# Optimization experiments

Hardware: AMD Instinct MI355X
Metric: run time of the kernel (lower is better)

## Reference

```python
import jax, jax.numpy as jnp
import numpy as np

FG_FRACTION = 0.5
FG_THRESH = 0.7
BG_HI = 0.5
BG_LO = 0.1
BATCHSIZE = 256
FG_ROIS = int(round(FG_FRACTION * BATCHSIZE))  # 128


def setup_inputs() -> dict:
    key = jax.random.key(0)
    k1, k2, k3 = jax.random.split(key, 3)
    N, K, C = 80000, 256, 81
    IMG = 800.0

    def make_boxes(k, n):
        ka, kb = jax.random.split(k)
        xy = jax.random.uniform(ka, (1, n, 2), dtype=jnp.float32) * (IMG - 136.0)
        wh = jax.random.uniform(kb, (1, n, 2), dtype=jnp.float32) * 128.0 + 8.0
        return jnp.concatenate([xy, xy + wh], axis=-1)  # valid x1<x2, y1<y2

    proposals = make_boxes(k1, N)          # (1, N, 4)
    gt_boxes = make_boxes(k2, K)           # (1, K, 4)
    cls = jax.random.randint(k3, (K,), 1, C)
    gt_labels = jax.nn.one_hot(cls, C, dtype=jnp.float32)[None]  # (1, K, C)
    return {"proposals": proposals, "gt_labels": gt_labels, "gt_boxes": gt_boxes}


def _iou(a, b):
    # a: (M,4), b: (K,4); keras_rcnn +1-pixel convention
    area_a = (a[:, 2] - a[:, 0] + 1.0) * (a[:, 3] - a[:, 1] + 1.0)
    area_b = (b[:, 2] - b[:, 0] + 1.0) * (b[:, 3] - b[:, 1] + 1.0)
    x1 = jnp.maximum(a[:, None, 0], b[None, :, 0])
    y1 = jnp.maximum(a[:, None, 1], b[None, :, 1])
    x2 = jnp.minimum(a[:, None, 2], b[None, :, 2])
    y2 = jnp.minimum(a[:, None, 3], b[None, :, 3])
    iw = jnp.maximum(x2 - x1 + 1.0, 0.0)
    ih = jnp.maximum(y2 - y1 + 1.0, 0.0)
    inter = iw * ih  # (M, K)
    return inter / (area_a[:, None] + area_b[None, :] - inter)


def _bbox_transform(ex, gt):
    ew = ex[:, 2] - ex[:, 0] + 1.0
    eh = ex[:, 3] - ex[:, 1] + 1.0
    ecx = ex[:, 0] + 0.5 * ew
    ecy = ex[:, 1] + 0.5 * eh
    gw = gt[:, 2] - gt[:, 0] + 1.0
    gh = gt[:, 3] - gt[:, 1] + 1.0
    gcx = gt[:, 0] + 0.5 * gw
    gcy = gt[:, 1] + 0.5 * gh
    return jnp.stack([(gcx - ecx) / ew, (gcy - ecy) / eh,
                      jnp.log(gw / ew), jnp.log(gh / eh)], axis=1)  # (B, 4)


def _forward(proposals, gt_labels, gt_boxes):
    all_rois = jnp.concatenate([proposals[0], gt_boxes[0]], axis=0)  # (M, 4)
    gt_b = gt_boxes[0]    # (K, 4)
    gt_l = gt_labels[0]   # (K, C)
    C = gt_l.shape[1]

    ov = _iou(all_rois, gt_b)               # (M, K)
    gt_assign = jnp.argmax(ov, axis=1)      # (M,)
    max_ov = jnp.max(ov, axis=1)            # (M,)

    fg_mask = max_ov >= FG_THRESH
    bg_mask = (max_ov < BG_HI) & (max_ov >= BG_LO)

    M = all_rois.shape[0]
    order = jnp.arange(M)
    # deterministic stand-in for random shuffle: candidates first, in index order
    fg_sorted = jnp.argsort(jnp.where(fg_mask, order, M + order))
    bg_sorted = jnp.argsort(jnp.where(bg_mask, order, M + order))
    num_fg = jnp.sum(fg_mask.astype(jnp.int32))
    fg_take = jnp.minimum(FG_ROIS, num_fg)

    pos = jnp.arange(BATCHSIZE)
    is_fg_slot = pos < fg_take
    keep = jnp.where(is_fg_slot,
                     fg_sorted[jnp.clip(pos, 0, M - 1)],
                     bg_sorted[jnp.clip(pos - fg_take, 0, M - 1)])  # (B,)

    rois = all_rois[keep]                    # (B, 4)
    labels = gt_l[gt_assign[keep]]           # (B, C)
    # set_label_background: bg slots -> one-hot class 0
    bg_onehot = jax.nn.one_hot(0, C, dtype=labels.dtype)
    labels = jnp.where(is_fg_slot[:, None], labels, bg_onehot[None, :])

    assigned_gt = gt_b[gt_assign[keep]]      # (B, 4)
    targets = _bbox_transform(rois, assigned_gt)  # (B, 4)

    # expand to N x 4K: only the argmax class (if > 0) gets nonzero targets
    clss = jnp.argmax(labels, axis=1)        # (B,)
    cls_oh = jnp.where((clss > 0)[:, None],
                       jax.nn.one_hot(clss, C, dtype=targets.dtype), 0.0)  # (B, C)
    bbox_targets = (cls_oh[:, :, None] * targets[:, None, :]).reshape(BATCHSIZE, 4 * C)

    return rois[None], labels[None], bbox_targets[None]


def reference(proposals, gt_labels, gt_boxes):
    return _forward(proposals, gt_labels, gt_boxes)
```

## Files before the change

kernel.cpp:

```cpp
#include <hip/hip_runtime.h>

#define FG_THRESH 0.7f
#define BG_HI 0.5f
#define BG_LO 0.1f
#define BATCH 256
#define FG_ROIS 128
#define KGT 256
#define CLS 81
#define CPT 5
#define NCHPAD 1280
#define NBIN 26
#define NSPAN 6

typedef unsigned long long ull;

__global__ __launch_bounds__(256) void k_iou(
    const float* __restrict__ proposals,
    const float* __restrict__ gt_boxes,
    int N, int M, int NCH,
    int* __restrict__ gt_assign,
    ull* __restrict__ fgm,
    ull* __restrict__ bgm,
    ull* __restrict__ nbm)
{
    __shared__ float4 gshE[KGT];
    __shared__ float garea[KGT];
    __shared__ ull pbx[4][NBIN], pby[4][NBIN];
    __shared__ ull intX[4][NBIN][NSPAN], intY[4][NBIN][NSPAN];
    __shared__ unsigned int wm[3][4];

    int tid = threadIdx.x;
    int wv = tid >> 6, lane = tid & 63;

    float4 g = ((const float4*)gt_boxes)[tid];
    gshE[tid] = g;
    garea[tid] = (g.z - g.x + 1.0f) * (g.w - g.y + 1.0f);

    for (int b = 0; b < NBIN; ++b) {
        float hiE = 32.0f * (float)(b + 1);
        float loE = 32.0f * (float)b - 1.0f;
        ull mx = __ballot((g.x < hiE) && (g.z > loE));
        ull my = __ballot((g.y < hiE) && (g.w > loE));
        if (lane == 0) { pbx[wv][b] = mx; pby[wv][b] = my; }
    }
    __syncthreads();

    if (tid < 104) {
        int c = tid / NBIN, b = tid % NBIN;
        ull m = pbx[c][b];
        intX[c][b][0] = m;
        #pragma unroll
        for (int s = 1; s < NSPAN; ++s) {
            int bb = b + s;
            if (bb < NBIN) m |= pbx[c][bb];
            intX[c][b][s] = m;
        }
    } else if (tid >= 128 && tid < 232) {
        int u = tid - 128;
        int c = u / NBIN, b = u % NBIN;
        ull m = pby[c][b];
        intY[c][b][0] = m;
        #pragma unroll
        for (int s = 1; s < NSPAN; ++s) {
            int bb = b + s;
            if (bb < NBIN) m |= pby[c][bb];
            intY[c][b][s] = m;
        }
    }
    __syncthreads();

    int c = lane & 3;
    int rj = lane >> 2;

    for (int p = 0; p < 2; ++p) {
        int ch = blockIdx.x * 2 + p;
        if (ch >= NCH) break;
        int roi = ch * 64 + wv * 16 + rj;
        bool val = (roi < M);

        float4 a;
        if (val) a = (roi < N) ? ((const float4*)proposals)[roi] : gshE[roi - N];
        else     a = gshE[0];
        float az1 = a.z + 1.0f, aw1 = a.w + 1.0f;
        float area_a = (a.z - a.x + 1.0f) * (a.w - a.y + 1.0f);

        int b1x = (int)(a.x * 0.03125f);
        int b2x = (int)(az1 * 0.03125f);
        int b1y = (int)(a.y * 0.03125f);
        int b2y = (int)(aw1 * 0.03125f);
        b2x = min(b2x, NBIN - 1); b2y = min(b2y, NBIN - 1);
        int sx = b2x - b1x;
        int sy = b2y - b1y;

        ull mbits = val ? (intX[c][b1x][sx] & intY[c][b1y][sy]) : 0ull;

        float best = 0.0f;
        int bestk = 0;
        while (mbits) {
            int j = __ffsll(mbits) - 1;
            mbits &= mbits - 1;
            int k = (c << 6) + j;
            float4 gg = gshE[k];
            float x1 = fmaxf(a.x, gg.x);
            float y1 = fmaxf(a.y, gg.y);
            float x2 = fminf(a.z, gg.z);
            float y2 = fminf(a.w, gg.w);
            float iw = fmaxf(x2 - x1 + 1.0f, 0.0f);
            float ih = fmaxf(y2 - y1 + 1.0f, 0.0f);
            float inter = iw * ih;
            float q = inter / (area_a + garea[k] - inter);
            if (q > best) { best = q; bestk = k; }
        }

        #pragma unroll
        for (int d = 1; d < 4; d <<= 1) {
            float ob = __shfl_xor(best, d);
            int   kb = __shfl_xor(bestk, d);
            if (ob > best || (ob == best && kb < bestk)) { best = ob; bestk = kb; }
        }
        float bset = __shfl(best, (lane & 15) * 4);
        int   bk   = __shfl(bestk, (lane & 15) * 4);

        int roi2 = ch * 64 + wv * 16 + (lane & 15);
        bool isv = (lane < 16) && (roi2 < M);
        bool fgp = isv && (bset >= FG_THRESH);
        bool bgp = isv && (bset < BG_HI) && (bset >= BG_LO);
        bool nbp = isv && !bgp;
        if (isv) gt_assign[roi2] = bk;

        unsigned int mf = (unsigned int)(__ballot(fgp) & 0xFFFFull);
        unsigned int mb = (unsigned int)(__ballot(bgp) & 0xFFFFull);
        unsigned int mn = (unsigned int)(__ballot(nbp) & 0xFFFFull);
        if (lane == 0) { wm[0][wv] = mf; wm[1][wv] = mb; wm[2][wv] = mn; }
        __syncthreads();
        if (tid == 0) {
            fgm[ch] = (ull)wm[0][0] | ((ull)wm[0][1] << 16) | ((ull)wm[0][2] << 32) | ((ull)wm[0][3] << 48);
            bgm[ch] = (ull)wm[1][0] | ((ull)wm[1][1] << 16) | ((ull)wm[1][2] << 32) | ((ull)wm[1][3] << 48);
            nbm[ch] = (ull)wm[2][0] | ((ull)wm[2][1] << 16) | ((ull)wm[2][2] << 32) | ((ull)wm[2][3] << 48);
        }
        __syncthreads();
    }
}

__global__ __launch_bounds__(256) void k_finish(
    const float* __restrict__ proposals,
    const float* __restrict__ gt_boxes,
    const float* __restrict__ gt_labels,
    int N, int NCH,
    const int* __restrict__ gt_assign,
    const ull* __restrict__ fgm,
    const ull* __restrict__ bgm,
    const ull* __restrict__ nbm,
    float* __restrict__ out_rois,
    float* __restrict__ out_labels,
    float4* __restrict__ out_bbox)
{
    __shared__ ull sf[NCHPAD], sb[NCHPAD], sn[NCHPAD];
    __shared__ int pf[NCHPAD], pb[NCHPAD], pn[NCHPAD];
    __shared__ int fgl[FG_ROIS], bgl[BATCH], nbl[BATCH];
    __shared__ int wtot[3][4];
    __shared__ int lm_cls[8];
    __shared__ float4 lm_t[8];

    int tid = threadIdx.x;
    int lane = tid & 63, wv = tid >> 6;

    for (int idx = tid; idx < NCHPAD; idx += 256) {
        bool v = (idx < NCH);
        sf[idx] = v ? fgm[idx] : 0ull;
        sb[idx] = v ? bgm[idx] : 0ull;
    }
    __syncthreads();

    int lo = tid * CPT;
    int pc0 = 0, pc1 = 0;
    #pragma unroll
    for (int r = 0; r < CPT; ++r) {
        pc0 += __popcll(sf[lo + r]);
        pc1 += __popcll(sb[lo + r]);
    }
    int i0 = pc0, i1 = pc1;
    #pragma unroll
    for (int d = 1; d < 64; d <<= 1) {
        int t0 = __shfl_up(i0, d);
        int t1 = __shfl_up(i1, d);
        if (lane >= d) { i0 += t0; i1 += t1; }
    }
    if (lane == 63) { wtot[0][wv] = i0; wtot[1][wv] = i1; }
    __syncthreads();
    int o0 = 0, o1 = 0;
    for (int x = 0; x < wv; ++x) { o0 += wtot[0][x]; o1 += wtot[1][x]; }
    int b0 = o0 + i0 - pc0;
    int b1 = o1 + i1 - pc1;
    int num_fg = wtot[0][0] + wtot[0][1] + wtot[0][2] + wtot[0][3];
    int num_bg = wtot[1][0] + wtot[1][1] + wtot[1][2] + wtot[1][3];
    int fg_take = min(FG_ROIS, num_fg);
    bool need_nb = (fg_take + num_bg < BATCH);

    #pragma unroll
    for (int r = 0; r < CPT; ++r) {
        int w = lo + r;
        pf[w] = b0; b0 += __popcll(sf[w]);
        pb[w] = b1; b1 += __popcll(sb[w]);
    }
    __syncthreads();

    #pragma unroll
    for (int pass = 0; pass < CPT; ++pass) {
        int w = tid + 256 * pass;
        int base = pf[w];
        if (base < FG_ROIS) {
            ull m = sf[w];
            while (m) {
                if (base >= FG_ROIS) break;
                fgl[base++] = (w << 6) + __ffsll(m) - 1;
                m &= m - 1;
            }
        }
        base = pb[w];
        if (base < BATCH) {
            ull m = sb[w];
            while (m) {
                if (base >= BATCH) break;
                bgl[base++] = (w << 6) + __ffsll(m) - 1;
                m &= m - 1;
            }
        }
    }

    if (need_nb) {
        for (int idx = tid; idx < NCHPAD; idx += 256) {
            sn[idx] = (idx < NCH) ? nbm[idx] : 0ull;
        }
        __syncthreads();
        int pc2 = 0;
        #pragma unroll
        for (int r = 0; r < CPT; ++r) pc2 += __popcll(sn[lo + r]);
        int i2 = pc2;
        #pragma unroll
        for (int d = 1; d < 64; d <<= 1) {
            int t2 = __shfl_up(i2, d);
            if (lane >= d) i2 += t2;
        }
        if (lane == 63) wtot[2][wv] = i2;
        __syncthreads();
        int o2 = 0;
        for (int x = 0; x < wv; ++x) o2 += wtot[2][x];
        int b2 = o2 + i2 - pc2;
        #pragma unroll
        for (int r = 0; r < CPT; ++r) {
            int w = lo + r;
            pn[w] = b2; b2 += __popcll(sn[w]);
        }
        __syncthreads();
        #pragma unroll
        for (int pass = 0; pass < CPT; ++pass) {
            int w = tid + 256 * pass;
            int base = pn[w];
            if (base < BATCH) {
                ull m = sn[w];
                while (m) {
                    if (base >= BATCH) break;
                    nbl[base++] = (w << 6) + __ffsll(m) - 1;
                    m &= m - 1;
                }
            }
        }
    }
    __syncthreads();

    int eBase = blockIdx.x * 256;
    int posLo = eBase / CLS;
    int posHi = (eBase + 255) / CLS;
    int np = posHi - posLo + 1;

    for (int s = wv; s < np; s += 4) {
        int pos = posLo + s;
        int is_fg = (pos < fg_take) ? 1 : 0;
        int j = pos - fg_take;
        int keep = is_fg ? fgl[pos] : ((j < num_bg) ? bgl[j] : nbl[j - num_bg]);
        float4 a = (keep < N) ? ((const float4*)proposals)[keep]
                              : ((const float4*)gt_boxes)[keep - N];
        int ga = gt_assign[keep];
        float4 g = ((const float4*)gt_boxes)[ga];

        float ew = a.z - a.x + 1.0f, eh = a.w - a.y + 1.0f;
        float ecx = a.x + 0.5f * ew, ecy = a.y + 0.5f * eh;
        float gw = g.z - g.x + 1.0f, gh = g.w - g.y + 1.0f;
        float gcx = g.x + 0.5f * gw, gcy = g.y + 0.5f * gh;

        int cls = 0;
        if (is_fg) {
            float l1 = gt_labels[(size_t)ga * CLS + lane];
            int c2 = lane + 64;
            float l2 = (c2 < CLS) ? gt_labels[(size_t)ga * CLS + c2] : 0.0f;
            ull m1 = __ballot(l1 > 0.5f);
            ull m2 = __ballot(c2 < CLS && l2 > 0.5f);
            cls = m1 ? (__ffsll(m1) - 1) : (m2 ? 64 + __ffsll(m2) - 1 : 0);
        }
        if (lane == 0) {
            lm_cls[s] = cls;
            lm_t[s] = make_float4((gcx - ecx) / ew, (gcy - ecy) / eh,
                                  logf(gw / ew), logf(gh / eh));
        }
    }

    if (blockIdx.x == 0) {
        int pos = tid;
        int is_fg = (pos < fg_take) ? 1 : 0;
        int j = pos - fg_take;
        int keep = is_fg ? fgl[pos] : ((j < num_bg) ? bgl[j] : nbl[j - num_bg]);
        float4 a = (keep < N) ? ((const float4*)proposals)[keep]
                              : ((const float4*)gt_boxes)[keep - N];
        ((float4*)out_rois)[pos] = a;
    }
    __syncthreads();

    int e = eBase + tid;
    int pos = e / CLS, cc = e - pos * CLS;
    int li = pos - posLo;
    int cl = lm_cls[li];
    out_labels[e] = (cc == cl) ? 1.0f : 0.0f;
    out_bbox[e] = (cl > 0 && cc == cl) ? lm_t[li]
                                       : make_float4(0.f, 0.f, 0.f, 0.f);
}

extern "C" void kernel_launch(void* const* d_in, const int* in_sizes, int n_in,
                              void* d_out, int out_size, void* d_ws, size_t ws_size,
                              hipStream_t stream)
{
    const float* proposals = (const float*)d_in[0];
    const float* gt_labels = (const float*)d_in[1];
    const float* gt_boxes  = (const float*)d_in[2];
    int N = in_sizes[0] / 4;
    int K = in_sizes[2] / 4;
    int M = N + K;
    int NCH = (M + 63) / 64;

    char* ws = (char*)d_ws;
    size_t off = 0;
    auto alloc = [&](size_t bytes) -> void* {
        void* p = ws + off;
        off += (bytes + 255) & ~(size_t)255;
        return p;
    };
    int* gt_assign = (int*)alloc((size_t)M * 4);
    ull* fgm = (ull*)alloc((size_t)NCH * 8);
    ull* bgm = (ull*)alloc((size_t)NCH * 8);
    ull* nbm = (ull*)alloc((size_t)NCH * 8);

    float* out_rois   = (float*)d_out;
    float* out_labels = out_rois + BATCH * 4;
    float4* out_bbox  = (float4*)(out_labels + BATCH * CLS);

    int nb1 = (NCH + 1) / 2;
    k_iou<<<nb1, 256, 0, stream>>>(proposals, gt_boxes, N, M, NCH,
                                   gt_assign, fgm, bgm, nbm);
    int nb2 = (BATCH * CLS) / 256;
    k_finish<<<nb2, 256, 0, stream>>>(proposals, gt_boxes, gt_labels, N, NCH,
                                      gt_assign, fgm, bgm, nbm,
                                      out_rois, out_labels, out_bbox);
    (void)K; (void)n_in; (void)out_size; (void)ws_size;
}
```

Before: 26.39 us.

## Assign one ROI per lane and one chunk per wave in IoU kernel

The IoU kernel now gives each lane a whole ROI, looping over all four GT groups itself, instead of spreading each ROI over four lanes and merging with shuffles. Each wave handles one 64-ROI chunk and writes its fg/bg/nb masks straight from a ballot, which removes the shared-memory staging and both block barriers per chunk. The grid is a quarter of the chunk count rather than half, so there are fewer blocks and less per-block setup of the bin tables. In exchange, each lane runs a longer serial loop over candidates, and lanes in a wave may diverge more because candidate counts differ per ROI.

```diff
diff --git a/kernel.cpp b/kernel.cpp
--- a/kernel.cpp
+++ b/kernel.cpp
@@ -27,7 +27,6 @@
     __shared__ float garea[KGT];
     __shared__ ull pbx[4][NBIN], pby[4][NBIN];
     __shared__ ull intX[4][NBIN][NSPAN], intY[4][NBIN][NSPAN];
-    __shared__ unsigned int wm[3][4];
 
     int tid = threadIdx.x;
     int wv = tid >> 6, lane = tid & 63;
@@ -69,33 +68,35 @@
     }
     __syncthreads();
 
-    int c = lane & 3;
-    int rj = lane >> 2;
-
-    for (int p = 0; p < 2; ++p) {
-        int ch = blockIdx.x * 2 + p;
-        if (ch >= NCH) break;
-        int roi = ch * 64 + wv * 16 + rj;
-        bool val = (roi < M);
-
-        float4 a;
-        if (val) a = (roi < N) ? ((const float4*)proposals)[roi] : gshE[roi - N];
-        else     a = gshE[0];
-        float az1 = a.z + 1.0f, aw1 = a.w + 1.0f;
-        float area_a = (a.z - a.x + 1.0f) * (a.w - a.y + 1.0f);
-
-        int b1x = (int)(a.x * 0.03125f);
-        int b2x = (int)(az1 * 0.03125f);
-        int b1y = (int)(a.y * 0.03125f);
-        int b2y = (int)(aw1 * 0.03125f);
-        b2x = min(b2x, NBIN - 1); b2y = min(b2y, NBIN - 1);
-        int sx = b2x - b1x;
-        int sy = b2y - b1y;
-
-        ull mbits = val ? (intX[c][b1x][sx] & intY[c][b1y][sy]) : 0ull;
-
-        float best = 0.0f;
-        int bestk = 0;
+    int ch = blockIdx.x * 4 + wv;
+    if (ch >= NCH) return;
+    int roi = ch * 64 + lane;
+    bool isv = (roi < M);
+
+    float4 a;
+    if (isv) a = (roi < N) ? ((const float4*)proposals)[roi] : gshE[roi - N];
+    else     a = gshE[0];
+    float az1 = a.z + 1.0f, aw1 = a.w + 1.0f;
+    float area_a = (a.z - a.x + 1.0f) * (a.w - a.y + 1.0f);
+
+    int b1x = (int)(a.x * 0.03125f);
+    int b2x = min((int)(az1 * 0.03125f), NBIN - 1);
+    int b1y = (int)(a.y * 0.03125f);
+    int b2y = min((int)(aw1 * 0.03125f), NBIN - 1);
+    int sx = b2x - b1x;
+    int sy = b2y - b1y;
+
+    ull m0 = intX[0][b1x][sx] & intY[0][b1y][sy];
+    ull m1 = intX[1][b1x][sx] & intY[1][b1y][sy];
+    ull m2 = intX[2][b1x][sx] & intY[2][b1y][sy];
+    ull m3 = intX[3][b1x][sx] & intY[3][b1y][sy];
+    if (!isv) { m0 = m1 = m2 = m3 = 0ull; }
+
+    float best = 0.0f;
+    int bestk = 0;
+    #pragma unroll
+    for (int c = 0; c < 4; ++c) {
+        ull mbits = (c == 0) ? m0 : (c == 1) ? m1 : (c == 2) ? m2 : m3;
         while (mbits) {
             int j = __ffsll(mbits) - 1;
             mbits &= mbits - 1;
@@ -111,35 +112,17 @@
             float q = inter / (area_a + garea[k] - inter);
             if (q > best) { best = q; bestk = k; }
         }
-
-        #pragma unroll
-        for (int d = 1; d < 4; d <<= 1) {
-            float ob = __shfl_xor(best, d);
-            int   kb = __shfl_xor(bestk, d);
-            if (ob > best || (ob == best && kb < bestk)) { best = ob; bestk = kb; }
-        }
-        float bset = __shfl(best, (lane & 15) * 4);
-        int   bk   = __shfl(bestk, (lane & 15) * 4);
-
-        int roi2 = ch * 64 + wv * 16 + (lane & 15);
-        bool isv = (lane < 16) && (roi2 < M);
-        bool fgp = isv && (bset >= FG_THRESH);
-        bool bgp = isv && (bset < BG_HI) && (bset >= BG_LO);
-        bool nbp = isv && !bgp;
-        if (isv) gt_assign[roi2] = bk;
-
-        unsigned int mf = (unsigned int)(__ballot(fgp) & 0xFFFFull);
-        unsigned int mb = (unsigned int)(__ballot(bgp) & 0xFFFFull);
-        unsigned int mn = (unsigned int)(__ballot(nbp) & 0xFFFFull);
-        if (lane == 0) { wm[0][wv] = mf; wm[1][wv] = mb; wm[2][wv] = mn; }
-        __syncthreads();
-        if (tid == 0) {
-            fgm[ch] = (ull)wm[0][0] | ((ull)wm[0][1] << 16) | ((ull)wm[0][2] << 32) | ((ull)wm[0][3] << 48);
-            bgm[ch] = (ull)wm[1][0] | ((ull)wm[1][1] << 16) | ((ull)wm[1][2] << 32) | ((ull)wm[1][3] << 48);
-            nbm[ch] = (ull)wm[2][0] | ((ull)wm[2][1] << 16) | ((ull)wm[2][2] << 32) | ((ull)wm[2][3] << 48);
-        }
-        __syncthreads();
-    }
+    }
+
+    bool fgp = isv && (best >= FG_THRESH);
+    bool bgp = isv && (best < BG_HI) && (best >= BG_LO);
+    bool nbp = isv && !bgp;
+    if (isv) gt_assign[roi] = bestk;
+
+    ull mf = __ballot(fgp);
+    ull mb = __ballot(bgp);
+    ull mn = __ballot(nbp);
+    if (lane == 0) { fgm[ch] = mf; bgm[ch] = mb; nbm[ch] = mn; }
 }
 
 __global__ __launch_bounds__(256) void k_finish(
@@ -353,7 +336,7 @@
     float* out_labels = out_rois + BATCH * 4;
     float4* out_bbox  = (float4*)(out_labels + BATCH * CLS);
 
-    int nb1 = (NCH + 1) / 2;
+    int nb1 = (NCH + 3) / 4;
     k_iou<<<nb1, 256, 0, stream>>>(proposals, gt_boxes, N, M, NCH,
                                    gt_assign, fgm, bgm, nbm);
     int nb2 = (BATCH * CLS) / 256;
```

After: 27.24 us. 3.2% more time.
